# Kernel tuning notes

Hardware: AMD Instinct MI355X
Metric: run time of the kernel (lower is better)

Reference implementation:

```python
import jax, jax.numpy as jnp
import numpy as np

NUM_ANCHORS = 3
NUM_CLASSES = 80
STRIDES = (16.0, 32.0)
ANCHORS = (
    jnp.array([[12.64, 19.39], [37.88, 51.48], [55.71, 138.31]], dtype=jnp.float32),
    jnp.array([[126.91, 78.23], [131.57, 214.55], [279.92, 258.87]], dtype=jnp.float32),
)


def conv1x1(x, w, b):
    # x: [B,C,H,W], w: [O,C], b: [O] -> [B,O,H,W]
    return jnp.einsum('bchw,oc->bohw', x, w) + b[None, :, None, None]


def decode_level(reg, obj, cls, stride, anchors):
    # reg: [B,12,H,W], obj: [B,3,H,W], cls: [B,80,H,W]
    B, _, H, W = reg.shape
    r = reg.transpose(0, 2, 3, 1).reshape(B, H, W, NUM_ANCHORS, 4)
    o = obj.transpose(0, 2, 3, 1).reshape(B, H, W, NUM_ANCHORS, 1)
    c = cls.transpose(0, 2, 3, 1)[:, :, :, None, :]  # [B,H,W,1,80], shared across anchors
    gy, gx = jnp.meshgrid(jnp.arange(H, dtype=reg.dtype), jnp.arange(W, dtype=reg.dtype), indexing='ij')
    grid = jnp.stack([gx, gy], axis=-1)[None, :, :, None, :]  # [1,H,W,1,2] = (x, y)
    xy = (jax.nn.sigmoid(r[..., :2]) * 2.0 - 0.5 + grid) * stride
    wh = (jax.nn.sigmoid(r[..., 2:4]) * 2.0) ** 2 * anchors  # anchors [3,2] broadcast
    ob = jax.nn.sigmoid(o)
    cp = jnp.broadcast_to(jax.nn.softmax(c, axis=-1), (B, H, W, NUM_ANCHORS, NUM_CLASSES))
    boxes = jnp.concatenate([xy, wh, ob, cp], axis=-1)  # [B,H,W,3,85]
    return boxes.reshape(B, H * W * NUM_ANCHORS, 5 + NUM_CLASSES)


def setup_inputs() -> dict:
    key = jax.random.key(0)
    ks = jax.random.split(key, 12)
    B, C = 64, 72
    inp = {
        'feat_reg0': jax.random.normal(ks[0], (B, C, 40, 40), jnp.float32),
        'feat_obj0': jax.random.normal(ks[1], (B, C, 40, 40), jnp.float32),
        'feat_cls0': jax.random.normal(ks[2], (B, C, 40, 40), jnp.float32),
        'feat_reg1': jax.random.normal(ks[3], (B, C, 20, 20), jnp.float32),
        'feat_obj1': jax.random.normal(ks[4], (B, C, 20, 20), jnp.float32),
        'feat_cls1': jax.random.normal(ks[5], (B, C, 20, 20), jnp.float32),
        'w_reg': jax.random.normal(ks[6], (4 * NUM_ANCHORS, C), jnp.float32) * 0.05,
        'b_reg': jax.random.normal(ks[7], (4 * NUM_ANCHORS,), jnp.float32) * 0.05,
        'w_obj': jax.random.normal(ks[8], (NUM_ANCHORS, C), jnp.float32) * 0.05,
        'b_obj': jax.random.normal(ks[9], (NUM_ANCHORS,), jnp.float32) * 0.05,
        'w_cls': jax.random.normal(ks[10], (NUM_CLASSES, C), jnp.float32) * 0.05,
        'b_cls': jax.random.normal(ks[11], (NUM_CLASSES,), jnp.float32) * 0.05,
    }
    return inp


def reference(feat_reg0, feat_obj0, feat_cls0, feat_reg1, feat_obj1, feat_cls1,
              w_reg, b_reg, w_obj, b_obj, w_cls, b_cls):
    feats = ((feat_reg0, feat_obj0, feat_cls0), (feat_reg1, feat_obj1, feat_cls1))
    outs = []
    for i, (fr, fo, fc) in enumerate(feats):
        reg = conv1x1(fr, w_reg, b_reg)
        obj = conv1x1(fo, w_obj, b_obj)
        cls = conv1x1(fc, w_cls, b_cls)
        outs.append(decode_level(reg, obj, cls, STRIDES[i], ANCHORS[i]))
    return jnp.concatenate(outs, axis=1)  # [B, 6000, 85]
```

## Files before the change

### kernel.cpp

```cpp
#include <hip/hip_runtime.h>
#include <math.h>

#define C_IN 72
#define RST 97
#define NFRAG 21
#define STG_T (16 * C_IN)
#define WF_BYTES (NFRAG * 64 * 16)
#define WAVE_LDS 6912

typedef short short8  __attribute__((ext_vector_type(8)));
typedef float floatx4 __attribute__((ext_vector_type(4)));

#define GLD4(dst, ptr) \
    asm volatile("global_load_dwordx4 %0, %1, off" : "=v"(dst) : "v"(ptr))

__device__ __forceinline__ unsigned short f2bf(float f) {
    unsigned u = __float_as_uint(f);
    u += 0x7FFFu + ((u >> 16) & 1u);
    return (unsigned short)(u >> 16);
}
__device__ __forceinline__ float sigf(float x) {
    return __builtin_amdgcn_rcpf(1.0f + __expf(-x));
}

__global__ void __launch_bounds__(256)
build_bfrags_kernel(const float* __restrict__ w_reg,
                    const float* __restrict__ w_obj,
                    const float* __restrict__ w_cls,
                    short8* __restrict__ frags)
{
    int idx = blockIdx.x * 256 + threadIdx.x;
    if (idx >= NFRAG * 64) return;
    int lane = idx & 63;
    int fi   = idx >> 6;
    int tile = fi / 3, kc = fi - tile * 3;
    int m = lane & 15, quad = lane >> 4;
    const float* wrow;
    bool valid = true;
    if (tile == 0)      { wrow = w_reg + m * C_IN; valid = (m < 12); }
    else if (tile == 1) { wrow = w_obj + m * C_IN; valid = (m < 3); }
    else                { wrow = w_cls + ((tile - 2) * 16 + m) * C_IN; }
    short8 r = {0, 0, 0, 0, 0, 0, 0, 0};
    if (valid && !(kc == 2 && quad != 0)) {
        const float* p = wrow + kc * 32 + quad * 8;
#pragma unroll
        for (int j = 0; j < 8; ++j) r[j] = (short)f2bf(p[j]);
    }
    frags[fi * 64 + lane] = r;
}

__global__ void __launch_bounds__(256)
yolo_head_kernel(const float* __restrict__ fr0, const float* __restrict__ fo0, const float* __restrict__ fc0,
                 const float* __restrict__ fr1, const float* __restrict__ fo1, const float* __restrict__ fc1,
                 const float* __restrict__ b_reg, const float* __restrict__ b_obj,
                 const float* __restrict__ b_cls,
                 const short8* __restrict__ wfrag,
                 float* __restrict__ out)
{
    __shared__ __align__(16) unsigned char smem[WF_BYTES + 4 * WAVE_LDS];
    short8* const wfl = (short8*)smem;
    const int tid  = threadIdx.x;
    const int wid  = tid >> 6;
    const int lane = tid & 63;
    unsigned short* const stage = (unsigned short*)(smem + WF_BYTES + wid * WAVE_LDS);
    float*          const row   = (float*)         (smem + WF_BYTES + wid * WAVE_LDS);

    for (int j = tid; j < NFRAG * 64; j += 256) wfl[j] = wfrag[j];
    __syncthreads();

    const int m    = lane & 15;
    const int quad = lane >> 4;
    const int chg  = lane >> 2;
    const int pg   = lane & 3;

    const int wg = blockIdx.x * 4 + wid;
    int lvl, HW, W, LO, sbase;
    const float *fr, *fo, *fc;
    if (wg < 1600) { lvl = 0; HW = 1600; W = 40; LO = 0;    sbase = wg * 4;
                     fr = fr0; fo = fo0; fc = fc0; }
    else           { lvl = 1; HW = 400;  W = 20; LO = 4800; sbase = (wg - 1600) * 4;
                     fr = fr1; fo = fo1; fc = fc1; }
    const float STRIDE = lvl ? 32.0f : 16.0f;
    const float* srcs[3] = {fr, fo, fc};

    const int a_ = m >> 2, k_ = m & 3;
    float anch;
    {
        float e0, e1;
        if (lvl == 0) { e0 = a_ == 0 ? 12.64f  : a_ == 1 ? 37.88f  : 55.71f;
                        e1 = a_ == 0 ? 19.39f  : a_ == 1 ? 51.48f  : 138.31f; }
        else          { e0 = a_ == 0 ? 126.91f : a_ == 1 ? 131.57f : 279.92f;
                        e1 = a_ == 0 ? 78.23f  : a_ == 1 ? 214.55f : 258.87f; }
        anch = (k_ == 3) ? e1 : e0;
    }
    const float brg = b_reg[m < 12 ? m : 0];
    const float bob = b_obj[m < 3 ? m : 0];
    float bcl[5];
#pragma unroll
    for (int nt = 0; nt < 5; ++nt) bcl[nt] = b_cls[nt * 16 + m];

    floatx4 ld[3][5];
    auto issueT1 = [&](int S) {
        int b, pos0;
        if (lvl == 0) { b = S / 100; pos0 = (S - b * 100) * 16; }
        else          { b = S / 25;  pos0 = (S - b * 25) * 16; }
        const int fb = b * C_IN * HW + pos0 + pg * 4;
#pragma unroll
        for (int t = 0; t < 3; ++t) {
            const float* sp = srcs[t] + fb;
#pragma unroll
            for (int g = 0; g < 4; ++g) {
                const float* p = sp + (g * 16 + chg) * HW;
                GLD4(ld[t][g], p);
            }
        }
        if (lane < 32) {
#pragma unroll
            for (int t = 0; t < 3; ++t) {
                const float* p = srcs[t] + fb + (64 + chg) * HW;
                GLD4(ld[t][4], p);
            }
        }
    };

    issueT1(sbase);

#pragma unroll
    for (int i = 0; i < 4; ++i) {
        const int S = sbase + i;
        int b, pos0;
        if (lvl == 0) { b = S / 100; pos0 = (S - b * 100) * 16; }
        else          { b = S / 25;  pos0 = (S - b * 25) * 16; }

        if (i == 0) asm volatile("s_waitcnt vmcnt(0)" ::: "memory");
        else        asm volatile("s_waitcnt vmcnt(16)" ::: "memory");
        __builtin_amdgcn_sched_barrier(0);

#pragma unroll
        for (int t = 0; t < 3; ++t) {
#pragma unroll
            for (int g = 0; g < 4; ++g)
#pragma unroll
                for (int ii = 0; ii < 4; ++ii)
                    stage[t * STG_T + (pg * 4 + ii) * C_IN + g * 16 + chg] = f2bf(ld[t][g][ii]);
            if (lane < 32)
#pragma unroll
                for (int ii = 0; ii < 4; ++ii)
                    stage[t * STG_T + (pg * 4 + ii) * C_IN + 64 + chg] = f2bf(ld[t][4][ii]);
        }
        asm volatile("s_waitcnt lgkmcnt(0)" ::: "memory");

        short8 af[3][3];
#pragma unroll
        for (int t = 0; t < 3; ++t) {
            const unsigned short* tp = stage + t * STG_T + m * C_IN;
            af[t][0] = *(const short8*)(tp + quad * 8);
            af[t][1] = *(const short8*)(tp + 32 + quad * 8);
            short8 v = *(const short8*)(tp + 64);
            if (quad) v = (short8){0, 0, 0, 0, 0, 0, 0, 0};
            af[t][2] = v;
        }
        asm volatile("s_waitcnt lgkmcnt(0)" ::: "memory");

        if (i < 3) issueT1(S + 1);

        floatx4 accR = {0, 0, 0, 0}, accO = {0, 0, 0, 0}, accC[5];
#pragma unroll
        for (int kc = 0; kc < 3; ++kc)
            accR = __builtin_amdgcn_mfma_f32_16x16x32_bf16(af[0][kc], wfl[(0 * 3 + kc) * 64 + lane], accR, 0, 0, 0);
#pragma unroll
        for (int kc = 0; kc < 3; ++kc)
            accO = __builtin_amdgcn_mfma_f32_16x16x32_bf16(af[1][kc], wfl[(1 * 3 + kc) * 64 + lane], accO, 0, 0, 0);
#pragma unroll
        for (int nt = 0; nt < 5; ++nt) {
            floatx4 a4 = {0, 0, 0, 0};
#pragma unroll
            for (int kc = 0; kc < 3; ++kc)
                a4 = __builtin_amdgcn_mfma_f32_16x16x32_bf16(af[2][kc], wfl[((nt + 2) * 3 + kc) * 64 + lane], a4, 0, 0, 0);
            accC[nt] = a4;
        }

#pragma unroll
        for (int ii = 0; ii < 4; ++ii) {
            const int prel = quad * 4 + ii;
            const int pg_  = pos0 + prel;
            const int gyi  = lvl ? (pg_ / 20) : (pg_ / 40);
            const float gx = (float)(pg_ - gyi * W);
            const float gy = (float)gyi;

            if (m < 12) {
                float sg = sigf(accR[ii] + brg);
                float v;
                if (k_ == 0)      v = (sg * 2.0f - 0.5f + gx) * STRIDE;
                else if (k_ == 1) v = (sg * 2.0f - 0.5f + gy) * STRIDE;
                else { float t2 = sg * 2.0f; v = t2 * t2 * anch; }
                row[prel * RST + a_ * 5 + k_] = v;
            }
            if (m < 3)
                row[prel * RST + m * 5 + 4] = sigf(accO[ii] + bob);

            float e[5];
            float s = 0.f;
#pragma unroll
            for (int nt = 0; nt < 5; ++nt) {
                e[nt] = __expf(accC[nt][ii] + bcl[nt]);
                s += e[nt];
            }
            s += __shfl_xor(s, 1, 16);
            s += __shfl_xor(s, 2, 16);
            s += __shfl_xor(s, 4, 16);
            s += __shfl_xor(s, 8, 16);
            const float inv = __builtin_amdgcn_rcpf(s);
#pragma unroll
            for (int nt = 0; nt < 5; ++nt)
                row[prel * RST + 15 + nt * 16 + m] = e[nt] * inv;
        }
        asm volatile("s_waitcnt lgkmcnt(0)" ::: "memory");

        float* outp = out + ((size_t)b * 510000 + LO * 85 + pos0 * 255);
#pragma unroll
        for (int s = 0; s < 16; ++s) {
            if (!(s == 15 && lane >= 60)) {
                floatx4 v;
#pragma unroll
                for (int j = 0; j < 4; ++j) {
                    const int F  = s * 256 + lane * 4 + j;
                    const int p  = (F * 4113) >> 20;
                    const int k  = F - p * 255;
                    const int a  = (k >= 85) + (k >= 170);
                    const int kk = k - a * 85;
                    const int wi = (kk < 5) ? (a * 5 + kk) : (15 + (kk - 5));
                    v[j] = row[p * RST + wi];
                }
                *(floatx4*)(outp + s * 256 + lane * 4) = v;
            }
        }
    }
}

extern "C" void kernel_launch(void* const* d_in, const int* in_sizes, int n_in,
                              void* d_out, int out_size, void* d_ws, size_t ws_size,
                              hipStream_t stream) {
    (void)in_sizes; (void)n_in; (void)ws_size; (void)out_size;
    const float* fr0  = (const float*)d_in[0];
    const float* fo0  = (const float*)d_in[1];
    const float* fc0  = (const float*)d_in[2];
    const float* fr1  = (const float*)d_in[3];
    const float* fo1  = (const float*)d_in[4];
    const float* fc1  = (const float*)d_in[5];
    const float* wreg = (const float*)d_in[6];
    const float* breg = (const float*)d_in[7];
    const float* wobj = (const float*)d_in[8];
    const float* bobj = (const float*)d_in[9];
    const float* wcls = (const float*)d_in[10];
    const float* bcls = (const float*)d_in[11];
    float* out = (float*)d_out;
    short8* frags = (short8*)d_ws;

    build_bfrags_kernel<<<6, 256, 0, stream>>>(wreg, wobj, wcls, frags);

    yolo_head_kernel<<<500, 256, 0, stream>>>(
        fr0, fo0, fc0, fr1, fo1, fc1,
        breg, bobj, bcls, frags, out);
}
```

Baseline: 257.1 us.

## Halve per-wave tiles, double grid, read weight fragments from global, swizzle blocks

Each wave now handles 2 position tiles instead of 4, and the grid doubles to 1000 blocks to raise parallelism and occupancy. The LDS copy of the weight fragments and its block barrier are removed, so MFMA B operands are read straight from global memory (through cache), which also shrinks LDS use per block. A blockIdx swizzle spreads consecutive blocks across XCDs. Trade-offs are more global weight loads inside the MFMA loop, a shorter software pipeline per wave, and a possible vmcnt accounting mismatch now that extra global loads are in flight.

```diff
diff --git a/kernel.cpp b/kernel.cpp
--- a/kernel.cpp
+++ b/kernel.cpp
@@ -5,7 +5,6 @@
 #define RST 97
 #define NFRAG 21
 #define STG_T (16 * C_IN)
-#define WF_BYTES (NFRAG * 64 * 16)
 #define WAVE_LDS 6912
 
 typedef short short8  __attribute__((ext_vector_type(8)));
@@ -57,31 +56,29 @@
                  const short8* __restrict__ wfrag,
                  float* __restrict__ out)
 {
-    __shared__ __align__(16) unsigned char smem[WF_BYTES + 4 * WAVE_LDS];
-    short8* const wfl = (short8*)smem;
+    __shared__ __align__(16) unsigned char smem[4 * WAVE_LDS];
     const int tid  = threadIdx.x;
     const int wid  = tid >> 6;
     const int lane = tid & 63;
-    unsigned short* const stage = (unsigned short*)(smem + WF_BYTES + wid * WAVE_LDS);
-    float*          const row   = (float*)         (smem + WF_BYTES + wid * WAVE_LDS);
-
-    for (int j = tid; j < NFRAG * 64; j += 256) wfl[j] = wfrag[j];
-    __syncthreads();
+    unsigned short* const stage = (unsigned short*)(smem + wid * WAVE_LDS);
+    float*          const row   = (float*)         (smem + wid * WAVE_LDS);
 
     const int m    = lane & 15;
     const int quad = lane >> 4;
     const int chg  = lane >> 2;
     const int pg   = lane & 3;
 
-    const int wg = blockIdx.x * 4 + wid;
-    int lvl, HW, W, LO, sbase;
-    const float *fr, *fo, *fc;
-    if (wg < 1600) { lvl = 0; HW = 1600; W = 40; LO = 0;    sbase = wg * 4;
-                     fr = fr0; fo = fo0; fc = fc0; }
-    else           { lvl = 1; HW = 400;  W = 20; LO = 4800; sbase = (wg - 1600) * 4;
-                     fr = fr1; fo = fo1; fc = fc1; }
+    const int swz   = (blockIdx.x & 7) * 125 + (blockIdx.x >> 3);
+    const int sbase = (swz * 4 + wid) * 2;
+    const int lvl   = (sbase >= 6400);
+    const int HW = lvl ? 400 : 1600;
+    const int W  = lvl ? 20 : 40;
+    const int LO = lvl ? 4800 : 0;
     const float STRIDE = lvl ? 32.0f : 16.0f;
-    const float* srcs[3] = {fr, fo, fc};
+    const float* srcs[3];
+    srcs[0] = lvl ? fr1 : fr0;
+    srcs[1] = lvl ? fo1 : fo0;
+    srcs[2] = lvl ? fc1 : fc0;
 
     const int a_ = m >> 2, k_ = m & 3;
     float anch;
@@ -101,9 +98,10 @@
 
     floatx4 ld[3][5];
     auto issueT1 = [&](int S) {
+        const int Sl = S - (lvl ? 6400 : 0);
         int b, pos0;
-        if (lvl == 0) { b = S / 100; pos0 = (S - b * 100) * 16; }
-        else          { b = S / 25;  pos0 = (S - b * 25) * 16; }
+        if (!lvl) { b = Sl / 100; pos0 = (Sl - b * 100) * 16; }
+        else      { b = Sl / 25;  pos0 = (Sl - b * 25) * 16; }
         const int fb = b * C_IN * HW + pos0 + pg * 4;
 #pragma unroll
         for (int t = 0; t < 3; ++t) {
@@ -126,11 +124,12 @@
     issueT1(sbase);
 
 #pragma unroll
-    for (int i = 0; i < 4; ++i) {
-        const int S = sbase + i;
+    for (int i = 0; i < 2; ++i) {
+        const int S  = sbase + i;
+        const int Sl = S - (lvl ? 6400 : 0);
         int b, pos0;
-        if (lvl == 0) { b = S / 100; pos0 = (S - b * 100) * 16; }
-        else          { b = S / 25;  pos0 = (S - b * 25) * 16; }
+        if (!lvl) { b = Sl / 100; pos0 = (Sl - b * 100) * 16; }
+        else      { b = Sl / 25;  pos0 = (Sl - b * 25) * 16; }
 
         if (i == 0) asm volatile("s_waitcnt vmcnt(0)" ::: "memory");
         else        asm volatile("s_waitcnt vmcnt(16)" ::: "memory");
@@ -162,21 +161,21 @@
         }
         asm volatile("s_waitcnt lgkmcnt(0)" ::: "memory");
 
-        if (i < 3) issueT1(S + 1);
+        if (i == 0) issueT1(S + 1);
 
         floatx4 accR = {0, 0, 0, 0}, accO = {0, 0, 0, 0}, accC[5];
 #pragma unroll
         for (int kc = 0; kc < 3; ++kc)
-            accR = __builtin_amdgcn_mfma_f32_16x16x32_bf16(af[0][kc], wfl[(0 * 3 + kc) * 64 + lane], accR, 0, 0, 0);
+            accR = __builtin_amdgcn_mfma_f32_16x16x32_bf16(af[0][kc], wfrag[(0 * 3 + kc) * 64 + lane], accR, 0, 0, 0);
 #pragma unroll
         for (int kc = 0; kc < 3; ++kc)
-            accO = __builtin_amdgcn_mfma_f32_16x16x32_bf16(af[1][kc], wfl[(1 * 3 + kc) * 64 + lane], accO, 0, 0, 0);
+            accO = __builtin_amdgcn_mfma_f32_16x16x32_bf16(af[1][kc], wfrag[(1 * 3 + kc) * 64 + lane], accO, 0, 0, 0);
 #pragma unroll
         for (int nt = 0; nt < 5; ++nt) {
             floatx4 a4 = {0, 0, 0, 0};
 #pragma unroll
             for (int kc = 0; kc < 3; ++kc)
-                a4 = __builtin_amdgcn_mfma_f32_16x16x32_bf16(af[2][kc], wfl[((nt + 2) * 3 + kc) * 64 + lane], a4, 0, 0, 0);
+                a4 = __builtin_amdgcn_mfma_f32_16x16x32_bf16(af[2][kc], wfrag[((nt + 2) * 3 + kc) * 64 + lane], a4, 0, 0, 0);
             accC[nt] = a4;
         }
 
@@ -259,7 +258,7 @@
 
     build_bfrags_kernel<<<6, 256, 0, stream>>>(wreg, wobj, wcls, frags);
 
-    yolo_head_kernel<<<500, 256, 0, stream>>>(
+    yolo_head_kernel<<<1000, 256, 0, stream>>>(
         fr0, fo0, fc0, fr1, fo1, fc1,
         breg, bobj, bcls, frags, out);
 }
```

Result: no change. 258.6 us (+0.6%).
